# Kernel optimization log

Measured on AMD Instinct MI355X. Metric: run time of the kernel, lower is better.

Reference implementation:

```python
import jax, jax.numpy as jnp
import numpy as np

CAPACITY_FACTOR = 1.2


def setup_inputs() -> dict:
    key = jax.random.key(0)
    k1, k2, k3 = jax.random.split(key, 3)
    B, S, D, E = 8, 4096, 512, 16
    x = jax.random.normal(k1, (B, S, D), dtype=jnp.float32)
    switch_w = jax.random.normal(k2, (E, D), dtype=jnp.float32) * 0.02
    switch_b = jnp.zeros((E,), dtype=jnp.float32)
    expert_w = jax.random.normal(k3, (E, D, D), dtype=jnp.float32) * 0.02
    expert_b = jnp.zeros((E, D), dtype=jnp.float32)
    return {"x": x, "switch_w": switch_w, "switch_b": switch_b,
            "expert_w": expert_w, "expert_b": expert_b}


def reference(x, switch_w, switch_b, expert_w, expert_b):
    B, S, D = x.shape
    E = switch_w.shape[0]
    N = B * S
    xf = x.reshape(N, D)

    # Router: softmax over experts, top-1 route.
    logits = xf @ switch_w.T + switch_b            # [N, E]
    probs = jax.nn.softmax(logits, axis=-1)
    route_probs = jnp.max(probs, axis=-1)          # [N]
    routes = jnp.argmax(probs, axis=-1)            # [N] int

    # Position of each token within its expert's queue (token order).
    oh = jax.nn.one_hot(routes, E, dtype=jnp.int32)            # [N, E]
    pos = jnp.take_along_axis(jnp.cumsum(oh, axis=0), routes[:, None], axis=1)[:, 0] - 1  # [N]

    capacity = int(CAPACITY_FACTOR * N / E)        # static
    keep = pos < capacity                          # [N] bool; overflow tokens dropped

    # Dispatch: scatter kept tokens into [E, capacity, D] buffer.
    # Out-of-capacity positions are out-of-bounds and dropped by scatter semantics.
    buf = jnp.zeros((E, capacity, D), dtype=xf.dtype).at[routes, pos].set(xf)

    # Per-expert Linear (torch Linear: y = x @ W.T + b), as one grouped GEMM.
    y = jnp.einsum('ecd,efd->ecf', buf, expert_w) + expert_b[:, None, :]  # [E, C, D]

    # Combine: gather expert outputs back; dropped tokens pass through x.
    gathered = y[routes, jnp.minimum(pos, capacity - 1)]       # [N, D]
    out = jnp.where(keep[:, None], gathered, xf) * route_probs[:, None]
    return out.reshape(B, S, D)
```

## Files before the change

### kernel.cpp

```cpp
#include <hip/hip_runtime.h>
#include <math.h>

#define N_TOK 32768
#define DIM   512
#define NEXP  16
#define CAP   2457
#define CAPP  2464
#define NCHUNK 512

typedef __attribute__((ext_vector_type(8))) short   short8;
typedef __attribute__((ext_vector_type(4))) short   short4v;
typedef __attribute__((ext_vector_type(4))) float   floatx4;

__device__ __forceinline__ short f2bf(float f) {
  unsigned u = __builtin_bit_cast(unsigned, f);
  unsigned r = u + 0x7FFFu + ((u >> 16) & 1u);
  return (short)(r >> 16);
}
__device__ __forceinline__ float bf2f(short h) {
  return __builtin_bit_cast(float, ((unsigned)(unsigned short)h) << 16);
}

#define LGP 17
__global__ __launch_bounds__(256) void router_k(
    const float* __restrict__ x, const float* __restrict__ sw,
    const float* __restrict__ sb, const float* __restrict__ ew,
    int* __restrict__ route, float* __restrict__ prob, int* __restrict__ hist,
    short* __restrict__ x_bf, short* __restrict__ w_bf) {
  __shared__ short swh[16][520];
  __shared__ short swl[16][520];
  __shared__ float lgt[64][LGP];
  __shared__ float sbs[NEXP];

  int tid = threadIdx.x;

  {
    const float4* src = (const float4*)ew;
    short4v* dst = (short4v*)w_bf;
    int base = blockIdx.x * 2048 + tid;
#pragma unroll
    for (int i = 0; i < 8; ++i) {
      float4 f = src[base + i * 256];
      short4v s;
      s[0] = f2bf(f.x); s[1] = f2bf(f.y); s[2] = f2bf(f.z); s[3] = f2bf(f.w);
      dst[base + i * 256] = s;
    }
  }

  {
    int idx = tid;
#pragma unroll
    for (int i = 0; i < 8; ++i, idx += 256) {
      int e = idx >> 7, k4 = idx & 127;
      float4 f = ((const float4*)(sw + e * DIM))[k4];
      short4v h, l;
      h[0] = f2bf(f.x); h[1] = f2bf(f.y); h[2] = f2bf(f.z); h[3] = f2bf(f.w);
      l[0] = f2bf(f.x - bf2f(h[0]));
      l[1] = f2bf(f.y - bf2f(h[1]));
      l[2] = f2bf(f.z - bf2f(h[2]));
      l[3] = f2bf(f.w - bf2f(h[3]));
      *(short4v*)&swh[e][k4 * 4] = h;
      *(short4v*)&swl[e][k4 * 4] = l;
    }
  }
  if (tid < NEXP) sbs[tid] = sb[tid];
  __syncthreads();

  int wv = tid >> 6, lane = tid & 63, q = lane >> 4, l16 = lane & 15;
  int row = blockIdx.x * 64 + wv * 16 + l16;
  const float* xr = x + (size_t)row * DIM;
  short* xbr = x_bf + (size_t)row * DIM;

  floatx4 acc = {};
#pragma unroll 4
  for (int kc = 0; kc < 16; ++kc) {
    int k0 = kc * 32 + q * 8;
    float4 f0 = *(const float4*)(xr + k0);
    float4 f1 = *(const float4*)(xr + k0 + 4);
    short8 hi, lo;
    hi[0] = f2bf(f0.x); hi[1] = f2bf(f0.y); hi[2] = f2bf(f0.z); hi[3] = f2bf(f0.w);
    hi[4] = f2bf(f1.x); hi[5] = f2bf(f1.y); hi[6] = f2bf(f1.z); hi[7] = f2bf(f1.w);
    lo[0] = f2bf(f0.x - bf2f(hi[0])); lo[1] = f2bf(f0.y - bf2f(hi[1]));
    lo[2] = f2bf(f0.z - bf2f(hi[2])); lo[3] = f2bf(f0.w - bf2f(hi[3]));
    lo[4] = f2bf(f1.x - bf2f(hi[4])); lo[5] = f2bf(f1.y - bf2f(hi[5]));
    lo[6] = f2bf(f1.z - bf2f(hi[6])); lo[7] = f2bf(f1.w - bf2f(hi[7]));
    *(short8*)(xbr + k0) = hi;
    short8 bh = *(const short8*)&swh[l16][k0];
    short8 bl = *(const short8*)&swl[l16][k0];
    acc = __builtin_amdgcn_mfma_f32_16x16x32_bf16(hi, bh, acc, 0, 0, 0);
    acc = __builtin_amdgcn_mfma_f32_16x16x32_bf16(lo, bh, acc, 0, 0, 0);
    acc = __builtin_amdgcn_mfma_f32_16x16x32_bf16(hi, bl, acc, 0, 0, 0);
    acc = __builtin_amdgcn_mfma_f32_16x16x32_bf16(lo, bl, acc, 0, 0, 0);
  }
#pragma unroll
  for (int r = 0; r < 4; ++r)
    lgt[wv * 16 + q * 4 + r][l16] = acc[r];
  __syncthreads();

  if (tid < 64) {
    int t = blockIdx.x * 64 + tid;
    float lg[NEXP];
#pragma unroll
    for (int e = 0; e < NEXP; ++e) lg[e] = lgt[tid][e] + sbs[e];
    int arg = 0; float mx = lg[0];
#pragma unroll
    for (int e = 1; e < NEXP; ++e)
      if (lg[e] > mx) { mx = lg[e]; arg = e; }
    float s = 0.f;
#pragma unroll
    for (int e = 0; e < NEXP; ++e) s += expf(lg[e] - mx);
    route[t] = arg;
    prob[t]  = 1.0f / s;
#pragma unroll
    for (int e = 0; e < NEXP; ++e) {
      unsigned long long m = __ballot(arg == e);
      if (tid == e) hist[blockIdx.x * NEXP + e] = __popcll(m);
    }
  }
}

__global__ __launch_bounds__(256) void scan_k(
    const int* __restrict__ hist, int* __restrict__ offs,
    int* __restrict__ counts) {
  __shared__ int part[16][NEXP];
  __shared__ int base[16][NEXP];
  int e = threadIdx.x & 15, g = threadIdx.x >> 4;
  int s = 0;
  for (int b = g * 32; b < g * 32 + 32; ++b) s += hist[b * NEXP + e];
  part[g][e] = s;
  __syncthreads();
  if (g == 0) {
    int run = 0;
#pragma unroll
    for (int gg = 0; gg < 16; ++gg) { base[gg][e] = run; run += part[gg][e]; }
    counts[e] = run;
  }
  __syncthreads();
  int run = base[g][e];
  for (int b = g * 32; b < g * 32 + 32; ++b) {
    offs[b * NEXP + e] = run;
    run += hist[b * NEXP + e];
  }
}

__global__ __launch_bounds__(64) void pos_k(
    const int* __restrict__ route, const float* __restrict__ prob,
    const int* __restrict__ offs, const float* __restrict__ x,
    float* __restrict__ out, int* __restrict__ lists) {
  int tid = threadIdx.x;
  int t = blockIdx.x * 64 + tid;
  int r = route[t];
  unsigned long long lower = (1ull << tid) - 1ull;
  int rank = 0;
#pragma unroll
  for (int e = 0; e < NEXP; ++e) {
    unsigned long long m = __ballot(r == e);
    if (r == e) rank = __popcll(m & lower);
  }
  int pos = offs[blockIdx.x * NEXP + r] + rank;
  if (pos < CAP) {
    lists[r * CAPP + pos] = t;
  } else {
    float p = prob[t];
    const float4* xr = (const float4*)(x + (size_t)t * DIM);
    float4* o = (float4*)(out + (size_t)t * DIM);
    for (int d = 0; d < DIM / 4; ++d) {
      float4 v = xr[d];
      v.x *= p; v.y *= p; v.z *= p; v.w *= p;
      o[d] = v;
    }
  }
}

#define BM 128
#define BN 128
#define BKS 64

__global__ __launch_bounds__(256, 2) void gemm_k(
    const short* __restrict__ x_bf, const short* __restrict__ w_bf,
    const float* __restrict__ eb, const int* __restrict__ lists,
    const int* __restrict__ counts, const float* __restrict__ prob,
    float* __restrict__ out) {
  int e = blockIdx.z;
  int cnt = counts[e]; if (cnt > CAP) cnt = CAP;
  int row0 = blockIdx.y * BM;
  if (row0 >= cnt) return;
  int col0 = blockIdx.x * BN;

  __shared__ short A_s[BM * BKS];
  __shared__ short B_s[BN * BKS];
  __shared__ int rowtok[BM];

  int tid = threadIdx.x;
  if (tid < BM) {
    int gr = row0 + tid;
    rowtok[tid] = (gr < cnt) ? lists[e * CAPP + gr] : 0;
  }
  __syncthreads();

  int wv = tid >> 6, lane = tid & 63;
  int q = lane >> 4, l16 = lane & 15;
  int wrow = (wv >> 1) * 64, wcol = (wv & 1) * 64;

  int r_loc = lane >> 3, c = lane & 7;
  int g = c ^ r_loc;
  const short* ga[4]; const short* gb[4];
  short* la[4]; short* lb[4];
#pragma unroll
  for (int t4 = 0; t4 < 4; ++t4) {
    int row = wv * 32 + t4 * 8 + r_loc;
    ga[t4] = x_bf + (size_t)rowtok[row] * DIM + g * 8;
    gb[t4] = w_bf + (size_t)(e * DIM + col0 + row) * DIM + g * 8;
    la[t4] = &A_s[(wv * 32 + t4 * 8) * BKS];
    lb[t4] = &B_s[(wv * 32 + t4 * 8) * BKS];
  }

  floatx4 acc[4][4] = {};

  for (int k0 = 0; k0 < DIM; k0 += BKS) {
#pragma unroll
    for (int t4 = 0; t4 < 4; ++t4) {
      __builtin_amdgcn_global_load_lds(
          (const __attribute__((address_space(1))) void*)(ga[t4] + k0),
          (__attribute__((address_space(3))) void*)(la[t4]), 16, 0, 0);
      __builtin_amdgcn_global_load_lds(
          (const __attribute__((address_space(1))) void*)(gb[t4] + k0),
          (__attribute__((address_space(3))) void*)(lb[t4]), 16, 0, 0);
    }
    __syncthreads();
#pragma unroll
    for (int kk = 0; kk < 2; ++kk) {
      short8 af[4], bfv[4];
      int ckbase = kk * 4 + q;
#pragma unroll
      for (int sm = 0; sm < 4; ++sm) {
        int row = wrow + sm * 16 + l16;
        int ph = ckbase ^ (row & 7);
        af[sm] = *(const short8*)&A_s[row * BKS + ph * 8];
      }
#pragma unroll
      for (int sn = 0; sn < 4; ++sn) {
        int row = wcol + sn * 16 + l16;
        int ph = ckbase ^ (row & 7);
        bfv[sn] = *(const short8*)&B_s[row * BKS + ph * 8];
      }
#pragma unroll
      for (int sm = 0; sm < 4; ++sm)
#pragma unroll
        for (int sn = 0; sn < 4; ++sn)
          acc[sm][sn] = __builtin_amdgcn_mfma_f32_16x16x32_bf16(
              af[sm], bfv[sn], acc[sm][sn], 0, 0, 0);
    }
    __syncthreads();
  }

#pragma unroll
  for (int sm = 0; sm < 4; ++sm) {
    int tt[4]; float pp[4]; int vld[4];
#pragma unroll
    for (int rg = 0; rg < 4; ++rg) {
      int rr = wrow + sm * 16 + q * 4 + rg;
      int gr = row0 + rr;
      vld[rg] = (gr < cnt);
      tt[rg]  = rowtok[rr];
      pp[rg]  = vld[rg] ? prob[tt[rg]] : 0.f;
    }
#pragma unroll
    for (int sn = 0; sn < 4; ++sn) {
      int col = col0 + wcol + sn * 16 + l16;
      float bias = eb[e * DIM + col];
#pragma unroll
      for (int rg = 0; rg < 4; ++rg)
        if (vld[rg])
          out[(size_t)tt[rg] * DIM + col] = (acc[sm][sn][rg] + bias) * pp[rg];
    }
  }
}

extern "C" void kernel_launch(void* const* d_in, const int* in_sizes, int n_in,
                              void* d_out, int out_size, void* d_ws, size_t ws_size,
                              hipStream_t stream) {
  const float* x  = (const float*)d_in[0];
  const float* sw = (const float*)d_in[1];
  const float* sb = (const float*)d_in[2];
  const float* ew = (const float*)d_in[3];
  const float* eb = (const float*)d_in[4];
  float* out = (float*)d_out;

  char* ws = (char*)d_ws;
  int*   route  = (int*)(ws + 0);
  float* prob   = (float*)(ws + 131072);
  int*   hist   = (int*)(ws + 262144);
  int*   offs   = (int*)(ws + 294912);
  int*   counts = (int*)(ws + 327680);
  int*   lists  = (int*)(ws + 327744);
  short* x_bf   = (short*)(ws + (1 << 20));
  short* w_bf   = (short*)(ws + (1 << 20) + 33554432);

  hipLaunchKernelGGL(router_k, dim3(NCHUNK), dim3(256), 0, stream,
                     x, sw, sb, ew, route, prob, hist, x_bf, w_bf);
  hipLaunchKernelGGL(scan_k, dim3(1), dim3(256), 0, stream, hist, offs, counts);
  hipLaunchKernelGGL(pos_k, dim3(NCHUNK), dim3(64), 0, stream,
                     route, prob, offs, x, out, lists);
  hipLaunchKernelGGL(gemm_k, dim3(4, 20, 16), dim3(256), 0, stream,
                     x_bf, w_bf, eb, lists, counts, prob, out);
}
```

Baseline: 184.7 us.

## Fuse scan into position kernel and halve GEMM row tile for occupancy

Removes the single-block scan kernel: each 256-thread position block now computes its own prefix over earlier chunk histograms and uses per-wave ballot counts for intra-block offsets, with the last block writing expert counts. The grouped GEMM drops to a 64-row tile with a launch bound of four blocks per SM and twice as many row blocks, aiming for better occupancy and less padding waste on partially filled expert tiles. It also fixes the LDS swizzle to use the row index. The trade-off is redundant histogram summation per block and less B-tile reuse per A row in the GEMM.

```diff
diff --git a/kernel.cpp b/kernel.cpp
--- a/kernel.cpp
+++ b/kernel.cpp
@@ -119,45 +119,45 @@
   }
 }
 
-__global__ __launch_bounds__(256) void scan_k(
-    const int* __restrict__ hist, int* __restrict__ offs,
+__global__ __launch_bounds__(256) void pos_k(
+    const int* __restrict__ route, const float* __restrict__ prob,
+    const int* __restrict__ hist, const float* __restrict__ x,
+    float* __restrict__ out, int* __restrict__ lists,
     int* __restrict__ counts) {
   __shared__ int part[16][NEXP];
-  __shared__ int base[16][NEXP];
-  int e = threadIdx.x & 15, g = threadIdx.x >> 4;
-  int s = 0;
-  for (int b = g * 32; b < g * 32 + 32; ++b) s += hist[b * NEXP + e];
-  part[g][e] = s;
-  __syncthreads();
-  if (g == 0) {
-    int run = 0;
-#pragma unroll
-    for (int gg = 0; gg < 16; ++gg) { base[gg][e] = run; run += part[gg][e]; }
-    counts[e] = run;
-  }
-  __syncthreads();
-  int run = base[g][e];
-  for (int b = g * 32; b < g * 32 + 32; ++b) {
-    offs[b * NEXP + e] = run;
-    run += hist[b * NEXP + e];
-  }
-}
-
-__global__ __launch_bounds__(64) void pos_k(
-    const int* __restrict__ route, const float* __restrict__ prob,
-    const int* __restrict__ offs, const float* __restrict__ x,
-    float* __restrict__ out, int* __restrict__ lists) {
+  __shared__ int base_s[NEXP];
+  __shared__ int wcnt[4][NEXP];
   int tid = threadIdx.x;
-  int t = blockIdx.x * 64 + tid;
+  int b = blockIdx.x;
+  int c0 = b * 4;
+  {
+    int g = tid >> 4, e = tid & 15;
+    int s = 0;
+    for (int c = g; c < c0; c += 16) s += hist[c * NEXP + e];
+    part[g][e] = s;
+  }
+  __syncthreads();
+  if (tid < NEXP) {
+    int s = 0;
+#pragma unroll
+    for (int gg = 0; gg < 16; ++gg) s += part[gg][tid];
+    base_s[tid] = s;
+  }
+  int wv = tid >> 6, lane = tid & 63;
+  int t = b * 256 + wv * 64 + lane;
   int r = route[t];
-  unsigned long long lower = (1ull << tid) - 1ull;
+  unsigned long long lower = (1ull << lane) - 1ull;
   int rank = 0;
 #pragma unroll
   for (int e = 0; e < NEXP; ++e) {
     unsigned long long m = __ballot(r == e);
     if (r == e) rank = __popcll(m & lower);
-  }
-  int pos = offs[blockIdx.x * NEXP + r] + rank;
+    if (lane == e) wcnt[wv][e] = __popcll(m);
+  }
+  __syncthreads();
+  int pre = base_s[r];
+  for (int w2 = 0; w2 < wv; ++w2) pre += wcnt[w2][r];
+  int pos = pre + rank;
   if (pos < CAP) {
     lists[r * CAPP + pos] = t;
   } else {
@@ -170,13 +170,16 @@
       o[d] = v;
     }
   }
-}
-
-#define BM 128
+  if (b == 127 && tid < NEXP)
+    counts[tid] = base_s[tid] + wcnt[0][tid] + wcnt[1][tid]
+                + wcnt[2][tid] + wcnt[3][tid];
+}
+
+#define BM 64
 #define BN 128
 #define BKS 64
 
-__global__ __launch_bounds__(256, 2) void gemm_k(
+__global__ __launch_bounds__(256, 4) void gemm_k(
     const short* __restrict__ x_bf, const short* __restrict__ w_bf,
     const float* __restrict__ eb, const int* __restrict__ lists,
     const int* __restrict__ counts, const float* __restrict__ prob,
@@ -200,40 +203,46 @@
 
   int wv = tid >> 6, lane = tid & 63;
   int q = lane >> 4, l16 = lane & 15;
-  int wrow = (wv >> 1) * 64, wcol = (wv & 1) * 64;
+  int wrow = (wv >> 1) * 32, wcol = (wv & 1) * 64;
 
   int r_loc = lane >> 3, c = lane & 7;
-  int g = c ^ r_loc;
-  const short* ga[4]; const short* gb[4];
-  short* la[4]; short* lb[4];
+  const short* ga[2]; short* la[2];
+  const short* gb[4]; short* lb[4];
+#pragma unroll
+  for (int t2 = 0; t2 < 2; ++t2) {
+    int row = wv * 16 + t2 * 8 + r_loc;
+    int g = c ^ (row & 7);
+    ga[t2] = x_bf + (size_t)rowtok[row] * DIM + g * 8;
+    la[t2] = &A_s[(wv * 16 + t2 * 8) * BKS];
+  }
 #pragma unroll
   for (int t4 = 0; t4 < 4; ++t4) {
     int row = wv * 32 + t4 * 8 + r_loc;
-    ga[t4] = x_bf + (size_t)rowtok[row] * DIM + g * 8;
+    int g = c ^ (row & 7);
     gb[t4] = w_bf + (size_t)(e * DIM + col0 + row) * DIM + g * 8;
-    la[t4] = &A_s[(wv * 32 + t4 * 8) * BKS];
     lb[t4] = &B_s[(wv * 32 + t4 * 8) * BKS];
   }
 
-  floatx4 acc[4][4] = {};
+  floatx4 acc[2][4] = {};
 
   for (int k0 = 0; k0 < DIM; k0 += BKS) {
 #pragma unroll
-    for (int t4 = 0; t4 < 4; ++t4) {
+    for (int t2 = 0; t2 < 2; ++t2)
       __builtin_amdgcn_global_load_lds(
-          (const __attribute__((address_space(1))) void*)(ga[t4] + k0),
-          (__attribute__((address_space(3))) void*)(la[t4]), 16, 0, 0);
+          (const __attribute__((address_space(1))) void*)(ga[t2] + k0),
+          (__attribute__((address_space(3))) void*)(la[t2]), 16, 0, 0);
+#pragma unroll
+    for (int t4 = 0; t4 < 4; ++t4)
       __builtin_amdgcn_global_load_lds(
           (const __attribute__((address_space(1))) void*)(gb[t4] + k0),
           (__attribute__((address_space(3))) void*)(lb[t4]), 16, 0, 0);
-    }
     __syncthreads();
 #pragma unroll
     for (int kk = 0; kk < 2; ++kk) {
-      short8 af[4], bfv[4];
+      short8 af[2], bfv[4];
       int ckbase = kk * 4 + q;
 #pragma unroll
-      for (int sm = 0; sm < 4; ++sm) {
+      for (int sm = 0; sm < 2; ++sm) {
         int row = wrow + sm * 16 + l16;
         int ph = ckbase ^ (row & 7);
         af[sm] = *(const short8*)&A_s[row * BKS + ph * 8];
@@ -245,7 +254,7 @@
         bfv[sn] = *(const short8*)&B_s[row * BKS + ph * 8];
       }
 #pragma unroll
-      for (int sm = 0; sm < 4; ++sm)
+      for (int sm = 0; sm < 2; ++sm)
 #pragma unroll
         for (int sn = 0; sn < 4; ++sn)
           acc[sm][sn] = __builtin_amdgcn_mfma_f32_16x16x32_bf16(
@@ -255,7 +264,7 @@
   }
 
 #pragma unroll
-  for (int sm = 0; sm < 4; ++sm) {
+  for (int sm = 0; sm < 2; ++sm) {
     int tt[4]; float pp[4]; int vld[4];
 #pragma unroll
     for (int rg = 0; rg < 4; ++rg) {
@@ -291,7 +300,6 @@
   int*   route  = (int*)(ws + 0);
   float* prob   = (float*)(ws + 131072);
   int*   hist   = (int*)(ws + 262144);
-  int*   offs   = (int*)(ws + 294912);
   int*   counts = (int*)(ws + 327680);
   int*   lists  = (int*)(ws + 327744);
   short* x_bf   = (short*)(ws + (1 << 20));
@@ -299,9 +307,8 @@
 
   hipLaunchKernelGGL(router_k, dim3(NCHUNK), dim3(256), 0, stream,
                      x, sw, sb, ew, route, prob, hist, x_bf, w_bf);
-  hipLaunchKernelGGL(scan_k, dim3(1), dim3(256), 0, stream, hist, offs, counts);
-  hipLaunchKernelGGL(pos_k, dim3(NCHUNK), dim3(64), 0, stream,
-                     route, prob, offs, x, out, lists);
-  hipLaunchKernelGGL(gemm_k, dim3(4, 20, 16), dim3(256), 0, stream,
+  hipLaunchKernelGGL(pos_k, dim3(128), dim3(256), 0, stream,
+                     route, prob, hist, x, out, lists, counts);
+  hipLaunchKernelGGL(gemm_k, dim3(4, 39, 16), dim3(256), 0, stream,
                      x_bf, w_bf, eb, lists, counts, prob, out);
 }
```

After: 183.6 us. About the same (-0.6%).
